# Kernel tuning notes

Hardware: AMD Instinct MI355X
Metric: run time of the kernel (lower is better)

## Reference

```python
import jax, jax.numpy as jnp
import numpy as np

NUM_SAMPLES = 64
PE_FREQS = 10
HIDDEN = 256
IN_PE = 3 + 3 * 2 * PE_FREQS  # 63


def positional_encoding(x):
    # x: [..., 3] -> [..., 63]
    freqs = 2.0 ** jnp.arange(PE_FREQS, dtype=x.dtype)  # [L]
    xb = x[..., None, :] * freqs[:, None]               # [..., L, 3]
    enc = jnp.concatenate([jnp.sin(xb), jnp.cos(xb)], axis=-1)  # [..., L, 6]
    return jnp.concatenate([x, enc.reshape(*x.shape[:-1], -1)], axis=-1)


def setup_inputs() -> dict:
    key = jax.random.key(0)
    ks = jax.random.split(key, 12)
    origins = jax.random.normal(ks[0], (2048, 3), dtype=jnp.float32)
    directions = jax.random.normal(ks[1], (2048, 3), dtype=jnp.float32)
    directions = directions / jnp.linalg.norm(directions, axis=-1, keepdims=True)

    def lin(kw, kb, fan_in, fan_out):
        s = 1.0 / np.sqrt(fan_in)
        W = jax.random.uniform(kw, (fan_in, fan_out), jnp.float32, -s, s)
        b = jax.random.uniform(kb, (fan_out,), jnp.float32, -s, s)
        return W, b

    W0, b0 = lin(ks[2], ks[3], IN_PE, HIDDEN)
    W1, b1 = lin(ks[4], ks[5], HIDDEN, HIDDEN)
    W2, b2 = lin(ks[6], ks[7], HIDDEN, HIDDEN)
    W3, b3 = lin(ks[8], ks[9], HIDDEN, 4)
    return {"origins": origins, "directions": directions,
            "near": 2.0, "far": 6.0,
            "W0": W0, "b0": b0, "W1": W1, "b1": b1,
            "W2": W2, "b2": b2, "W3": W3, "b3": b3}


def field_mlp(x, W0, b0, W1, b1, W2, b2, W3, b3):
    h = positional_encoding(x)
    h = jax.nn.relu(h @ W0 + b0)
    h = jax.nn.relu(h @ W1 + b1)
    h = jax.nn.relu(h @ W2 + b2)
    return h @ W3 + b3  # [..., 4]


def reference(origins, directions, near, far, W0, b0, W1, b1, W2, b2, W3, b3):
    near = jnp.float32(near)
    far = jnp.float32(far)
    # 1) sample generation (faithful to source, including its midpoint formula)
    boundaries = jnp.linspace(near, far, NUM_SAMPLES + 1)          # [S+1]
    midpoints = boundaries[:-1] + boundaries[1:] / 2               # [S] (as in source)
    samples = jnp.einsum('i,jk->jik', midpoints, directions)      # [B,S,3]
    locations = origins[:, None, :] + samples                      # [B,S,3]
    # 2) field eval (vectorized; equivalent to per-ray list comprehension)
    field_out = field_mlp(locations, W0, b0, W1, b1, W2, b2, W3, b3)  # [B,S,4]
    rgb = jax.nn.sigmoid(field_out[..., :3])                       # [B,S,3]
    sigma = jax.nn.relu(field_out[..., 3])                         # [B,S]
    # 3) alpha values
    delta = jnp.diff(boundaries)                                    # [S]
    alpha = 1.0 - jnp.exp(-sigma * delta)                           # [B,S]
    # 4) alpha composite: exclusive cumprod transmittance (O(N) form of source loop)
    trans = jnp.cumprod(1.0 - alpha, axis=1)
    T = jnp.concatenate([jnp.ones_like(alpha[:, :1]), trans[:, :-1]], axis=1)
    weights = T * alpha                                             # [B,S]
    return jnp.sum(weights[..., None] * rgb, axis=1)                # [B,3]
```

## Files before the change

### kernel.cpp

```cpp
#include <hip/hip_runtime.h>
#include <math.h>

typedef _Float16 h8 __attribute__((ext_vector_type(8)));
typedef _Float16 h4 __attribute__((ext_vector_type(4)));
typedef float    f4 __attribute__((ext_vector_type(4)));

#define SAMPLES 64
#define HIDDEN  256

#define OFF_W0 0
#define OFF_W1 16384
#define OFF_W2 81920
#define OFF_W3 147456

__launch_bounds__(256)
__global__ void prep_weights(const float* __restrict__ W0,
                             const float* __restrict__ W1,
                             const float* __restrict__ W2,
                             const float* __restrict__ W3,
                             _Float16* __restrict__ ws)
{
    const int ln = threadIdx.x & 63;
    const int t  = blockIdx.x * 4 + (threadIdx.x >> 6);
    if (t >= 296) return;

    const float* src; int off, kg, ct, kmax, colmax, wide;
    if (t < 32)       { src=W0; off=OFF_W0; kg=t>>4;        ct=t&15;        kmax=63;  colmax=256; wide=1; }
    else if (t < 160) { int u=t-32;  src=W1; off=OFF_W1; kg=u>>4; ct=u&15; kmax=256; colmax=256; wide=1; }
    else if (t < 288) { int u=t-160; src=W2; off=OFF_W2; kg=u>>4; ct=u&15; kmax=256; colmax=256; wide=1; }
    else              { int u=t-288; src=W3; off=OFF_W3; kg=u;    ct=0;    kmax=256; colmax=4;   wide=0; }

    const int col = ct*16 + (ln & 15);
    const int k0  = kg*32 + ((ln >> 4) << 3);
    h8 vh;
#pragma unroll
    for (int j = 0; j < 8; ++j) {
        int k = k0 + j;
        float v = (k < kmax && col < colmax) ? src[k*colmax + col] : 0.0f;
        vh[j] = (_Float16)v;
    }
    int di = wide ? ((kg*16 + ct)*64 + ln) : (kg*64 + ln);
    ((h8*)(ws + off))[di] = vh;
}

template<int NKG>
__device__ __forceinline__ void dense_layer(const _Float16* __restrict__ W,
                                            const float*    __restrict__ bias,
                                            _Float16* B, int wv, int lane)
{
    const int q  = lane >> 4;
    const int jl = lane & 15;
    f4 acc[2][8];
#pragma unroll
    for (int cht = 0; cht < 2; ++cht) {
        f4 bb = ((const f4*)bias)[wv*8 + cht*4 + q];
#pragma unroll
        for (int st = 0; st < 8; ++st) acc[cht][st] = bb;
    }
    const h8* wp = (const h8*)W;
    const h8* bp = (const h8*)B;

    h8 ca[2];
#pragma unroll
    for (int cht = 0; cht < 2; ++cht)
        ca[cht] = wp[(wv*2 + cht)*64 + lane];

#pragma unroll
    for (int kg = 0; kg < NKG; ++kg) {
        h8 na[2];
        int kn = (kg + 1 < NKG) ? kg + 1 : kg;
#pragma unroll
        for (int cht = 0; cht < 2; ++cht)
            na[cht] = wp[(kn*16 + wv*2 + cht)*64 + lane];
#pragma unroll
        for (int st = 0; st < 8; ++st) {
            h8 bh = bp[(kg*8 + st)*64 + lane];
            acc[0][st] = __builtin_amdgcn_mfma_f32_16x16x32_f16(ca[0], bh, acc[0][st], 0, 0, 0);
            acc[1][st] = __builtin_amdgcn_mfma_f32_16x16x32_f16(ca[1], bh, acc[1][st], 0, 0, 0);
        }
        ca[0] = na[0]; ca[1] = na[1];
    }

    __syncthreads();

#pragma unroll
    for (int cht = 0; cht < 2; ++cht) {
        int lnp = jl + 16*(cht*2 + (q >> 1));
        int jb  = (q & 1)*4;
#pragma unroll
        for (int st = 0; st < 8; ++st) {
            h4 vh;
#pragma unroll
            for (int r = 0; r < 4; ++r)
                vh[r] = (_Float16)fmaxf(acc[cht][st][r], 0.0f);
            *(h4*)(B + ((wv*8 + st)*64 + lnp)*8 + jb) = vh;
        }
    }
    __syncthreads();
}

__launch_bounds__(512, 2)
__global__ void nerf_fused(const float* __restrict__ origins,
                           const float* __restrict__ dirs,
                           const float* __restrict__ nearp,
                           const float* __restrict__ farp,
                           const float* __restrict__ b0,
                           const float* __restrict__ b1,
                           const float* __restrict__ b2,
                           const float* __restrict__ b3,
                           const _Float16* __restrict__ ws,
                           float* __restrict__ out,
                           int nrays)
{
    extern __shared__ _Float16 sm[];
    _Float16* B = sm;
    float* headv = (float*)(sm + 32768);

    const int tid  = threadIdx.x;
    const int wv   = tid >> 6;
    const int lane = tid & 63;
    const int ray0 = blockIdx.x * 2;
    const int ray1 = ray0 + 1;
    const int ray1c = (ray1 < nrays) ? ray1 : (nrays - 1);

    const float near = nearp[0];
    const float far  = farp[0];
    const float step = (far - near) * (1.0f / 64.0f);

    const float o0x = origins[ray0*3+0], o0y = origins[ray0*3+1], o0z = origins[ray0*3+2];
    const float d0x = dirs[ray0*3+0],    d0y = dirs[ray0*3+1],    d0z = dirs[ray0*3+2];
    const float o1x = origins[ray1c*3+0], o1y = origins[ray1c*3+1], o1z = origins[ray1c*3+2];
    const float d1x = dirs[ray1c*3+0],    d1y = dirs[ray1c*3+1],    d1z = dirs[ray1c*3+2];

#pragma unroll
    for (int half = 0; half < 2; ++half) {
        int b  = tid + half*512;
        int ln = b & 63;
        int st = (b >> 6) & 7;
        int rr = st >> 2;
        int sample = (st & 3)*16 + (ln & 15);
        int k0 = (b >> 9)*32 + ((ln >> 4) << 3);
        float mid = (near + (float)sample*step) + (near + (float)(sample+1)*step)*0.5f;
        float cox = rr ? o1x : o0x, coy = rr ? o1y : o0y, coz = rr ? o1z : o0z;
        float cdx = rr ? d1x : d0x, cdy = rr ? d1y : d0y, cdz = rr ? d1z : d0z;
        float c3[3] = { cox + mid*cdx, coy + mid*cdy, coz + mid*cdz };
        h8 vh;
#pragma unroll
        for (int j = 0; j < 8; ++j) {
            int k = k0 + j;
            float v;
            if (k < 3) v = c3[k];
            else if (k < 63) {
                int t = k - 3, l = t/6, r = t%6, d = r%3;
                float a = c3[d] * (float)(1 << l);
                v = (r < 3) ? sinf(a) : cosf(a);
            } else v = 0.0f;
            vh[j] = (_Float16)v;
        }
        ((h8*)B)[b] = vh;
    }
    __syncthreads();

    dense_layer<2>(ws+OFF_W0, b0, B, wv, lane);
    dense_layer<8>(ws+OFF_W1, b1, B, wv, lane);
    dense_layer<8>(ws+OFF_W2, b2, B, wv, lane);

    f4 hacc[8];
    {
        h8 ah = ((const h8*)(ws+OFF_W3))[wv*64 + lane];
        const h8* bp = (const h8*)B;
#pragma unroll
        for (int st = 0; st < 8; ++st) {
            f4 z = (f4){0.f, 0.f, 0.f, 0.f};
            hacc[st] = __builtin_amdgcn_mfma_f32_16x16x32_f16(ah, bp[(wv*8 + st)*64 + lane], z, 0, 0, 0);
        }
    }
    __syncthreads();

    f4* part = (f4*)sm;
#pragma unroll
    for (int st = 0; st < 8; ++st) part[(wv*8 + st)*64 + lane] = hacc[st];
    __syncthreads();

    {
        int stt = tid >> 6, l = tid & 63;
        f4 s = part[(0*8 + stt)*64 + l];
#pragma unroll
        for (int w = 1; w < 8; ++w) s += part[(w*8 + stt)*64 + l];
        int q = l >> 4, jl = l & 15;
        if (q == 0) {
            s += *(const f4*)b3;
            ((f4*)headv)[(stt >> 2)*64 + (stt & 3)*16 + jl] = s;
        }
    }
    __syncthreads();

    if (tid < 128) {
        const int rr = tid >> 6;
        const int p  = tid & 63;
        f4 f = ((const f4*)headv)[rr*64 + p];
        float sigma = fmaxf(f[3], 0.0f);
        float delta = (near + (float)(p + 1)*step) - (near + (float)p*step);
        float alpha = 1.0f - expf(-sigma * delta);
        float om    = 1.0f - alpha;

        float prod = om;
#pragma unroll
        for (int off = 1; off < 64; off <<= 1) {
            float v = __shfl_up(prod, off, 64);
            if (p >= off) prod *= v;
        }
        float T = __shfl_up(prod, 1, 64);
        if (p == 0) T = 1.0f;
        float w = T * alpha;

        float r  = w * (1.0f / (1.0f + expf(-f[0])));
        float g  = w * (1.0f / (1.0f + expf(-f[1])));
        float bb = w * (1.0f / (1.0f + expf(-f[2])));
#pragma unroll
        for (int off = 32; off > 0; off >>= 1) {
            r  += __shfl_down(r,  off, 64);
            g  += __shfl_down(g,  off, 64);
            bb += __shfl_down(bb, off, 64);
        }
        if (p == 0 && ray0 + rr < nrays) {
            out[(ray0 + rr)*3 + 0] = r;
            out[(ray0 + rr)*3 + 1] = g;
            out[(ray0 + rr)*3 + 2] = bb;
        }
    }
}

extern "C" void kernel_launch(void* const* d_in, const int* in_sizes, int n_in,
                              void* d_out, int out_size, void* d_ws, size_t ws_size,
                              hipStream_t stream) {
    const float* origins = (const float*)d_in[0];
    const float* dirs    = (const float*)d_in[1];
    const float* nearp   = (const float*)d_in[2];
    const float* farp    = (const float*)d_in[3];
    const float* W0      = (const float*)d_in[4];
    const float* b0      = (const float*)d_in[5];
    const float* W1      = (const float*)d_in[6];
    const float* b1      = (const float*)d_in[7];
    const float* W2      = (const float*)d_in[8];
    const float* b2      = (const float*)d_in[9];
    const float* W3      = (const float*)d_in[10];
    const float* b3      = (const float*)d_in[11];
    float* out           = (float*)d_out;
    _Float16* ws         = (_Float16*)d_ws;

    const int nrays = in_sizes[0] / 3;
    const int nblk  = (nrays + 1) / 2;

    prep_weights<<<dim3(74), dim3(256), 0, stream>>>(W0, W1, W2, W3, ws);

    const size_t shmem = 32768 * sizeof(_Float16) + 128 * sizeof(f4);
    hipFuncSetAttribute(reinterpret_cast<const void*>(nerf_fused),
                        hipFuncAttributeMaxDynamicSharedMemorySize,
                        (int)shmem);
    nerf_fused<<<dim3(nblk), dim3(512), shmem, stream>>>(
        origins, dirs, nearp, farp, b0, b1, b2, b3, ws, out, nrays);
}
```

Baseline: 140.2 us.

## Prefetch next-layer weights across layers and compute PE via double-angle recurrence

Weight fragments for the next layer are now prefetched during the last k-group of the current layer and carried in registers across layer boundaries, including into the head layer. The bias add moves from accumulator initialization to the epilogue, and LDS B-fragment reads are batched four at a time before their MFMAs. Positional encoding now computes sin/cos once per coordinate and derives higher frequencies with double-angle recurrences, with each thread producing two fragments. This cuts transcendental work but can accumulate rounding error at high frequencies compared with direct sinf/cosf.

```diff
diff --git a/kernel.cpp b/kernel.cpp
--- a/kernel.cpp
+++ b/kernel.cpp
@@ -46,45 +46,56 @@
 template<int NKG>
 __device__ __forceinline__ void dense_layer(const _Float16* __restrict__ W,
                                             const float*    __restrict__ bias,
-                                            _Float16* B, int wv, int lane)
+                                            _Float16* B, int wv, int lane,
+                                            h8 (&ca)[2],
+                                            const h8* __restrict__ next0,
+                                            const h8* __restrict__ next1)
 {
     const int q  = lane >> 4;
     const int jl = lane & 15;
     f4 acc[2][8];
 #pragma unroll
-    for (int cht = 0; cht < 2; ++cht) {
-        f4 bb = ((const f4*)bias)[wv*8 + cht*4 + q];
-#pragma unroll
-        for (int st = 0; st < 8; ++st) acc[cht][st] = bb;
-    }
+    for (int cht = 0; cht < 2; ++cht)
+#pragma unroll
+        for (int st = 0; st < 8; ++st) acc[cht][st] = (f4){0.f, 0.f, 0.f, 0.f};
+
     const h8* wp = (const h8*)W;
     const h8* bp = (const h8*)B;
 
-    h8 ca[2];
-#pragma unroll
-    for (int cht = 0; cht < 2; ++cht)
-        ca[cht] = wp[(wv*2 + cht)*64 + lane];
-
 #pragma unroll
     for (int kg = 0; kg < NKG; ++kg) {
         h8 na[2];
-        int kn = (kg + 1 < NKG) ? kg + 1 : kg;
-#pragma unroll
-        for (int cht = 0; cht < 2; ++cht)
-            na[cht] = wp[(kn*16 + wv*2 + cht)*64 + lane];
-#pragma unroll
-        for (int st = 0; st < 8; ++st) {
-            h8 bh = bp[(kg*8 + st)*64 + lane];
-            acc[0][st] = __builtin_amdgcn_mfma_f32_16x16x32_f16(ca[0], bh, acc[0][st], 0, 0, 0);
-            acc[1][st] = __builtin_amdgcn_mfma_f32_16x16x32_f16(ca[1], bh, acc[1][st], 0, 0, 0);
+        if (kg + 1 < NKG) {
+#pragma unroll
+            for (int cht = 0; cht < 2; ++cht)
+                na[cht] = wp[((kg+1)*16 + wv*2 + cht)*64 + lane];
+        } else {
+            na[0] = *next0;
+            na[1] = *next1;
+        }
+#pragma unroll
+        for (int sh = 0; sh < 2; ++sh) {
+            h8 bh[4];
+#pragma unroll
+            for (int s = 0; s < 4; ++s)
+                bh[s] = bp[(kg*8 + sh*4 + s)*64 + lane];
+#pragma unroll
+            for (int s = 0; s < 4; ++s) {
+                acc[0][sh*4+s] = __builtin_amdgcn_mfma_f32_16x16x32_f16(ca[0], bh[s], acc[0][sh*4+s], 0, 0, 0);
+                acc[1][sh*4+s] = __builtin_amdgcn_mfma_f32_16x16x32_f16(ca[1], bh[s], acc[1][sh*4+s], 0, 0, 0);
+            }
         }
         ca[0] = na[0]; ca[1] = na[1];
     }
 
+    f4 bb0 = ((const f4*)bias)[wv*8 + q];
+    f4 bb1 = ((const f4*)bias)[wv*8 + 4 + q];
+
     __syncthreads();
 
 #pragma unroll
     for (int cht = 0; cht < 2; ++cht) {
+        f4 bb = cht ? bb1 : bb0;
         int lnp = jl + 16*(cht*2 + (q >> 1));
         int jb  = (q & 1)*4;
 #pragma unroll
@@ -92,7 +103,7 @@
             h4 vh;
 #pragma unroll
             for (int r = 0; r < 4; ++r)
-                vh[r] = (_Float16)fmaxf(acc[cht][st][r], 0.0f);
+                vh[r] = (_Float16)fmaxf(acc[cht][st][r] + bb[r], 0.0f);
             *(h4*)(B + ((wv*8 + st)*64 + lnp)*8 + jb) = vh;
         }
     }
@@ -123,51 +134,102 @@
     const int ray1 = ray0 + 1;
     const int ray1c = (ray1 < nrays) ? ray1 : (nrays - 1);
 
+    const int fi0 = (wv*2 + 0)*64 + lane;
+    const int fi1 = (wv*2 + 1)*64 + lane;
+    const h8* w0p = (const h8*)(ws + OFF_W0);
+    const h8* w1p = (const h8*)(ws + OFF_W1);
+    const h8* w2p = (const h8*)(ws + OFF_W2);
+    const h8* w3p = (const h8*)(ws + OFF_W3);
+    h8 wca[2];
+    wca[0] = w0p[fi0];
+    wca[1] = w0p[fi1];
+
     const float near = nearp[0];
     const float far  = farp[0];
     const float step = (far - near) * (1.0f / 64.0f);
 
-    const float o0x = origins[ray0*3+0], o0y = origins[ray0*3+1], o0z = origins[ray0*3+2];
-    const float d0x = dirs[ray0*3+0],    d0y = dirs[ray0*3+1],    d0z = dirs[ray0*3+2];
-    const float o1x = origins[ray1c*3+0], o1y = origins[ray1c*3+1], o1z = origins[ray1c*3+2];
-    const float d1x = dirs[ray1c*3+0],    d1y = dirs[ray1c*3+1],    d1z = dirs[ray1c*3+2];
-
-#pragma unroll
-    for (int half = 0; half < 2; ++half) {
-        int b  = tid + half*512;
-        int ln = b & 63;
-        int st = (b >> 6) & 7;
-        int rr = st >> 2;
-        int sample = (st & 3)*16 + (ln & 15);
-        int k0 = (b >> 9)*32 + ((ln >> 4) << 3);
-        float mid = (near + (float)sample*step) + (near + (float)(sample+1)*step)*0.5f;
-        float cox = rr ? o1x : o0x, coy = rr ? o1y : o0y, coz = rr ? o1z : o0z;
-        float cdx = rr ? d1x : d0x, cdy = rr ? d1y : d0y, cdz = rr ? d1z : d0z;
-        float c3[3] = { cox + mid*cdx, coy + mid*cdy, coz + mid*cdz };
-        h8 vh;
-#pragma unroll
-        for (int j = 0; j < 8; ++j) {
-            int k = k0 + j;
-            float v;
-            if (k < 3) v = c3[k];
-            else if (k < 63) {
-                int t = k - 3, l = t/6, r = t%6, d = r%3;
-                float a = c3[d] * (float)(1 << l);
-                v = (r < 3) ? sinf(a) : cosf(a);
-            } else v = 0.0f;
-            vh[j] = (_Float16)v;
-        }
-        ((h8*)B)[b] = vh;
-    }
-    __syncthreads();
-
-    dense_layer<2>(ws+OFF_W0, b0, B, wv, lane);
-    dense_layer<8>(ws+OFF_W1, b1, B, wv, lane);
-    dense_layer<8>(ws+OFF_W2, b2, B, wv, lane);
+    {
+        const int f  = tid >> 7;
+        const int sg = tid & 127;
+        const int rr = sg >> 6;
+        const int p  = sg & 63;
+        const int st = rr*4 + (p >> 4);
+        const int jl = p & 15;
+        const int kg = f >> 1;
+        const int q0 = (f & 1)*2;
+
+        const float mid = (near + (float)p*step) + (near + (float)(p+1)*step)*0.5f;
+        const float ox = origins[ray0*3+0], oy = origins[ray0*3+1], oz = origins[ray0*3+2];
+        const float dx = dirs[ray0*3+0],    dy = dirs[ray0*3+1],    dz = dirs[ray0*3+2];
+        const float o1x = origins[ray1c*3+0], o1y = origins[ray1c*3+1], o1z = origins[ray1c*3+2];
+        const float d1x = dirs[ray1c*3+0],    d1y = dirs[ray1c*3+1],    d1z = dirs[ray1c*3+2];
+        float c3[3];
+        c3[0] = (rr ? o1x : ox) + mid*(rr ? d1x : dx);
+        c3[1] = (rr ? o1y : oy) + mid*(rr ? d1y : dy);
+        c3[2] = (rr ? o1z : oz) + mid*(rr ? d1z : dz);
+
+        float ls0 = sinf(c3[0]), lc0 = cosf(c3[0]);
+        float ls1 = sinf(c3[1]), lc1 = cosf(c3[1]);
+        float ls2 = sinf(c3[2]), lc2 = cosf(c3[2]);
+#define DBL() { float t0 = 2.f*ls0*lc0; lc0 = 1.f - 2.f*ls0*ls0; ls0 = t0; \
+                float t1 = 2.f*ls1*lc1; lc1 = 1.f - 2.f*ls1*ls1; ls1 = t1; \
+                float t2 = 2.f*ls2*lc2; lc2 = 1.f - 2.f*ls2*ls2; ls2 = t2; }
+        h8 vh0, vh1;
+        if (f == 0) {
+            vh0[0]=(_Float16)c3[0]; vh0[1]=(_Float16)c3[1]; vh0[2]=(_Float16)c3[2];
+            vh0[3]=(_Float16)ls0;   vh0[4]=(_Float16)ls1;   vh0[5]=(_Float16)ls2;
+            vh0[6]=(_Float16)lc0;   vh0[7]=(_Float16)lc1;   vh1[0]=(_Float16)lc2;
+            DBL();
+            vh1[1]=(_Float16)ls0; vh1[2]=(_Float16)ls1; vh1[3]=(_Float16)ls2;
+            vh1[4]=(_Float16)lc0; vh1[5]=(_Float16)lc1; vh1[6]=(_Float16)lc2;
+            DBL();
+            vh1[7]=(_Float16)ls0;
+        } else if (f == 1) {
+            DBL(); DBL();
+            vh0[0]=(_Float16)ls1; vh0[1]=(_Float16)ls2;
+            vh0[2]=(_Float16)lc0; vh0[3]=(_Float16)lc1; vh0[4]=(_Float16)lc2;
+            DBL();
+            vh0[5]=(_Float16)ls0; vh0[6]=(_Float16)ls1; vh0[7]=(_Float16)ls2;
+            vh1[0]=(_Float16)lc0; vh1[1]=(_Float16)lc1; vh1[2]=(_Float16)lc2;
+            DBL();
+            vh1[3]=(_Float16)ls0; vh1[4]=(_Float16)ls1; vh1[5]=(_Float16)ls2;
+            vh1[6]=(_Float16)lc0; vh1[7]=(_Float16)lc1;
+        } else if (f == 2) {
+            DBL(); DBL(); DBL(); DBL();
+            vh0[0]=(_Float16)lc2;
+            DBL();
+            vh0[1]=(_Float16)ls0; vh0[2]=(_Float16)ls1; vh0[3]=(_Float16)ls2;
+            vh0[4]=(_Float16)lc0; vh0[5]=(_Float16)lc1; vh0[6]=(_Float16)lc2;
+            DBL();
+            vh0[7]=(_Float16)ls0; vh1[0]=(_Float16)ls1; vh1[1]=(_Float16)ls2;
+            vh1[2]=(_Float16)lc0; vh1[3]=(_Float16)lc1; vh1[4]=(_Float16)lc2;
+            DBL();
+            vh1[5]=(_Float16)ls0; vh1[6]=(_Float16)ls1; vh1[7]=(_Float16)ls2;
+        } else {
+            DBL(); DBL(); DBL(); DBL(); DBL(); DBL(); DBL();
+            vh0[0]=(_Float16)lc0; vh0[1]=(_Float16)lc1; vh0[2]=(_Float16)lc2;
+            DBL();
+            vh0[3]=(_Float16)ls0; vh0[4]=(_Float16)ls1; vh0[5]=(_Float16)ls2;
+            vh0[6]=(_Float16)lc0; vh0[7]=(_Float16)lc1; vh1[0]=(_Float16)lc2;
+            DBL();
+            vh1[1]=(_Float16)ls0; vh1[2]=(_Float16)ls1; vh1[3]=(_Float16)ls2;
+            vh1[4]=(_Float16)lc0; vh1[5]=(_Float16)lc1; vh1[6]=(_Float16)lc2;
+            vh1[7]=(_Float16)0.0f;
+        }
+#undef DBL
+        ((h8*)B)[(kg*8 + st)*64 + (q0    )*16 + jl] = vh0;
+        ((h8*)B)[(kg*8 + st)*64 + (q0 + 1)*16 + jl] = vh1;
+    }
+    __syncthreads();
+
+    dense_layer<2>(ws+OFF_W0, b0, B, wv, lane, wca, &w1p[fi0], &w1p[fi1]);
+    dense_layer<8>(ws+OFF_W1, b1, B, wv, lane, wca, &w2p[fi0], &w2p[fi1]);
+    dense_layer<8>(ws+OFF_W2, b2, B, wv, lane, wca,
+                   &w3p[wv*64 + lane], &w3p[wv*64 + lane]);
 
     f4 hacc[8];
     {
-        h8 ah = ((const h8*)(ws+OFF_W3))[wv*64 + lane];
+        h8 ah = wca[0];
         const h8* bp = (const h8*)B;
 #pragma unroll
         for (int st = 0; st < 8; ++st) {
```

Measured after the change: 118.3 us, median of 4. 15.6% less time.
